# Optimization experiments

Measured on AMD Instinct MI355X. Metric: run time of the kernel, lower is better.

Reference implementation:

```python
import jax, jax.numpy as jnp
import numpy as np

N_NODES = 100000
N_EDGES = 640000
D_FEAT = 128
N_HIDDEN = 32


def setup_inputs() -> dict:
    key = jax.random.key(0)
    ks = jax.random.split(key, 8)
    x = jax.random.normal(ks[0], (N_NODES, D_FEAT), dtype=jnp.float32)
    edge_index = jax.random.randint(ks[1], (2, N_EDGES), 0, N_NODES, dtype=jnp.int64)
    # Glorot-ish scaled params
    W1_l = jax.random.normal(ks[2], (D_FEAT, N_HIDDEN), dtype=jnp.float32) / np.sqrt(D_FEAT)
    W1_r = jax.random.normal(ks[3], (D_FEAT, N_HIDDEN), dtype=jnp.float32) / np.sqrt(D_FEAT)
    b1 = jnp.zeros((N_HIDDEN,), dtype=jnp.float32)
    W2_l = jax.random.normal(ks[4], (N_HIDDEN, 1), dtype=jnp.float32) / np.sqrt(N_HIDDEN)
    W2_r = jax.random.normal(ks[5], (N_HIDDEN, 1), dtype=jnp.float32) / np.sqrt(N_HIDDEN)
    b2 = jnp.zeros((1,), dtype=jnp.float32)
    return {"x": x, "edge_index": edge_index, "W1_l": W1_l, "W1_r": W1_r,
            "b1": b1, "W2_l": W2_l, "W2_r": W2_r, "b2": b2}


def _sage_conv(h, src, dst, n_nodes, W_l, W_r, b):
    # mean aggregation of source features at destination nodes (PyG SAGEConv default)
    msg_sum = jax.ops.segment_sum(h[src], dst, num_segments=n_nodes)          # [N, d]
    deg = jax.ops.segment_sum(jnp.ones_like(src, dtype=h.dtype), dst,
                              num_segments=n_nodes)                           # [N]
    mean = msg_sum / jnp.maximum(deg, 1.0)[:, None]
    return mean @ W_l + h @ W_r + b


def reference(x, edge_index, W1_l, W1_r, b1, W2_l, W2_r, b2):
    src, dst = edge_index[0], edge_index[1]
    n = x.shape[0]
    h = jax.nn.relu(_sage_conv(x, src, dst, n, W1_l, W1_r, b1))
    # dropout p=0.1 is identity at inference (training=False)
    out = _sage_conv(h, src, dst, n, W2_l, W2_r, b2)
    return out  # [N, 1] node logits
```

## Files before the change

kernel.cpp:

```cpp
#include <hip/hip_runtime.h>

#define NN 100000
#define NE 640000
#define DF 128
#define NH 32
#define CAP 32
#define BINS 1563
#define BCAP 768
#define HBLK 256
#define EPB 2500
#define NTILE 6250
#define GEMMB 1563

typedef __attribute__((ext_vector_type(8))) short bf16x8;
typedef __attribute__((ext_vector_type(4))) float f32x4;

__device__ __forceinline__ unsigned short f2bf(float x) {
    union { float f; unsigned u; } c; c.f = x;
    unsigned r = c.u + 0x7fffu + ((c.u >> 16) & 1u);
    return (unsigned short)(r >> 16);
}
__device__ __forceinline__ float bf2f(unsigned short b) {
    union { unsigned u; float f; } c; c.u = ((unsigned)b) << 16;
    return c.f;
}

__global__ __launch_bounds__(256) void gemm_hist_kernel(
    const float* __restrict__ x, const float* __restrict__ W1_l,
    const float* __restrict__ W1_r, unsigned short* __restrict__ xl_bf,
    unsigned short* __restrict__ xr_bf, const int* __restrict__ dst,
    int* __restrict__ histmat)
{
    __shared__ unsigned short wl[8192];

    if (blockIdx.x >= GEMMB) {
        int* lh = (int*)wl;
        const int h = blockIdx.x - GEMMB;
        for (int b = threadIdx.x; b < BINS; b += 256) lh[b] = 0;
        __syncthreads();
        const int e0 = h * EPB;
        for (int i = threadIdx.x; i < EPB; i += 256)
            atomicAdd(&lh[dst[e0 + i] >> 6], 1);
        __syncthreads();
        for (int b = threadIdx.x; b < BINS; b += 256)
            histmat[b * HBLK + h] = lh[b];
        return;
    }

    for (int s = threadIdx.x; s < 1024; s += 256) {
        int lane = s & 63;
        int nt = (s >> 6) & 3;
        int ks = s >> 8;
        int n = nt * 16 + (lane & 15);
        const float* Wc = (n < 32) ? (W1_l + n) : (W1_r + (n - 32));
        unsigned short v[8];
#pragma unroll
        for (int i = 0; i < 8; i++) {
            int k = ks * 32 + ((i >> 2) << 4) + ((lane >> 4) << 2) + (i & 3);
            v[i] = f2bf(Wc[(size_t)k * 32]);
        }
        unsigned u0 = (unsigned)v[0] | ((unsigned)v[1] << 16);
        unsigned u1 = (unsigned)v[2] | ((unsigned)v[3] << 16);
        unsigned u2 = (unsigned)v[4] | ((unsigned)v[5] << 16);
        unsigned u3 = (unsigned)v[6] | ((unsigned)v[7] << 16);
        *(uint4*)&wl[s * 8] = make_uint4(u0, u1, u2, u3);
    }
    __syncthreads();

    const int lane = threadIdx.x & 63;
    const int tile = (blockIdx.x << 2) + (threadIdx.x >> 6);
    if (tile >= NTILE) return;
    const int m = lane & 15, g = lane >> 4;
    const int row0 = tile << 4;

#define BLOAD(ks, nt) const bf16x8 b##ks##nt = *(const bf16x8*)&wl[(((ks)*4 + (nt)) * 64 + lane) * 8];
    BLOAD(0,0) BLOAD(0,1) BLOAD(0,2) BLOAD(0,3)
    BLOAD(1,0) BLOAD(1,1) BLOAD(1,2) BLOAD(1,3)
    BLOAD(2,0) BLOAD(2,1) BLOAD(2,2) BLOAD(2,3)
    BLOAD(3,0) BLOAD(3,1) BLOAD(3,2) BLOAD(3,3)
#undef BLOAD

    f32x4 acc0 = {0.f,0.f,0.f,0.f}, acc1 = {0.f,0.f,0.f,0.f};
    f32x4 acc2 = {0.f,0.f,0.f,0.f}, acc3 = {0.f,0.f,0.f,0.f};

    const float* xp = x + (size_t)(row0 + m) * DF + g * 4;

#define KSTEP(ks) { \
    float4 fa = *(const float4*)(xp + (ks) * 32); \
    float4 fb = *(const float4*)(xp + (ks) * 32 + 16); \
    bf16x8 af; \
    af[0] = (short)f2bf(fa.x); af[1] = (short)f2bf(fa.y); \
    af[2] = (short)f2bf(fa.z); af[3] = (short)f2bf(fa.w); \
    af[4] = (short)f2bf(fb.x); af[5] = (short)f2bf(fb.y); \
    af[6] = (short)f2bf(fb.z); af[7] = (short)f2bf(fb.w); \
    acc0 = __builtin_amdgcn_mfma_f32_16x16x32_bf16(af, b##ks##0, acc0, 0, 0, 0); \
    acc1 = __builtin_amdgcn_mfma_f32_16x16x32_bf16(af, b##ks##1, acc1, 0, 0, 0); \
    acc2 = __builtin_amdgcn_mfma_f32_16x16x32_bf16(af, b##ks##2, acc2, 0, 0, 0); \
    acc3 = __builtin_amdgcn_mfma_f32_16x16x32_bf16(af, b##ks##3, acc3, 0, 0, 0); }
    KSTEP(0) KSTEP(1) KSTEP(2) KSTEP(3)
#undef KSTEP

#define CSTORE(nt) { \
    int n = (nt) * 16 + m; \
_Pragma("unroll") \
    for (int r = 0; r < 4; r++) { \
        int rr = row0 + g * 4 + r; \
        unsigned short v = f2bf(acc##nt[r]); \
        if (n < 32) xl_bf[(size_t)rr * 32 + n] = v; \
        else        xr_bf[(size_t)rr * 32 + (n - 32)] = v; \
    } }
    CSTORE(0) CSTORE(1) CSTORE(2) CSTORE(3)
#undef CSTORE
}

__global__ __launch_bounds__(256) void scan_kernel(const int* __restrict__ histmat,
                                                   int* __restrict__ startmat,
                                                   int* __restrict__ len)
{
    __shared__ int ls[256];
    const int j = blockIdx.x, t = threadIdx.x;
    int h = histmat[j * HBLK + t];
    ls[t] = h;
    __syncthreads();
    for (int off = 1; off < 256; off <<= 1) {
        int v = (t >= off) ? ls[t - off] : 0;
        __syncthreads();
        ls[t] += v;
        __syncthreads();
    }
    startmat[j * HBLK + t] = ls[t] - h;
    if (t == 255) len[j] = ls[255];
}

__global__ __launch_bounds__(256) void scatter_kernel(const int* __restrict__ src,
                                                      const int* __restrict__ dst,
                                                      const int* __restrict__ startmat,
                                                      int* __restrict__ binned)
{
    __shared__ int lhist[BINS];
    const int h = blockIdx.x;
    for (int b = threadIdx.x; b < BINS; b += 256) lhist[b] = 0;
    __syncthreads();
    const int e0 = h * EPB;
    for (int i = threadIdx.x; i < EPB; i += 256) {
        int s = src[e0 + i], d = dst[e0 + i];
        int bin = d >> 6;
        int lr = atomicAdd(&lhist[bin], 1);
        int pos = bin * BCAP + startmat[bin * HBLK + h] + lr;
        binned[pos] = (s << 6) | (d & 63);
    }
}

__global__ __launch_bounds__(256) void agg1_bin_kernel(
    const int* __restrict__ binned, const int* __restrict__ len,
    const unsigned short* __restrict__ xl_bf, const unsigned short* __restrict__ xr_bf,
    const float* __restrict__ b1, const float* __restrict__ W2_l,
    const float* __restrict__ W2_r, float* __restrict__ h2l, float* __restrict__ hrp)
{
    __shared__ int lcnt[64];
    __shared__ int lesrc[64 * CAP];
    const int j = blockIdx.x, t = threadIdx.x;
    if (t < 64) lcnt[t] = 0;
    __syncthreads();
    const int L = len[j];
    const int* seg = binned + (size_t)j * BCAP;
    for (int i = t; i < L; i += 256) {
        int pk = seg[i];
        int dl = pk & 63, s = pk >> 6;
        int p = atomicAdd(&lcnt[dl], 1);
        if (p < CAP) lesrc[(dl << 5) + p] = s;
    }
    __syncthreads();

    const int l = t & 31, grp = t >> 5;
    const int j8 = l >> 2, c = l & 3;
    const float4* b14 = (const float4*)&b1[c * 8];
    float4 bb0 = b14[0], bb1 = b14[1];
    const float4* wl4 = (const float4*)&W2_l[c * 8];
    float4 wl0 = wl4[0], wl1 = wl4[1];
    const float4* wr4 = (const float4*)&W2_r[c * 8];
    float4 wr0 = wr4[0], wr1 = wr4[1];
    const float bs[8]  = {bb0.x, bb0.y, bb0.z, bb0.w, bb1.x, bb1.y, bb1.z, bb1.w};
    const float wls[8] = {wl0.x, wl0.y, wl0.z, wl0.w, wl1.x, wl1.y, wl1.z, wl1.w};
    const float wrs[8] = {wr0.x, wr0.y, wr0.z, wr0.w, wr1.x, wr1.y, wr1.z, wr1.w};

    for (int dl = grp; dl < 64; dl += 8) {
        const int node = j * 64 + dl;
        if (node >= NN) break;
        const int dg = lcnt[dl];
        const int lim = (dg < CAP) ? dg : CAP;

        float acc[8];
#pragma unroll
        for (int i = 0; i < 8; i++) acc[i] = 0.f;

        for (int jb = 0; jb < lim; jb += 8) {
            int jj = jb + j8;
            if (jj < lim) {
                int s = lesrc[(dl << 5) + jj];
                uint4 v = *(const uint4*)&xl_bf[(size_t)s * NH + c * 8];
#pragma unroll
                for (int i = 0; i < 4; i++) {
                    unsigned u = (&v.x)[i];
                    acc[2 * i]     += bf2f((unsigned short)(u & 0xffffu));
                    acc[2 * i + 1] += bf2f((unsigned short)(u >> 16));
                }
            }
        }
#pragma unroll
        for (int mm = 4; mm <= 16; mm <<= 1)
#pragma unroll
            for (int i = 0; i < 8; i++) acc[i] += __shfl_xor(acc[i], mm);

        const float inv = 1.0f / fmaxf((float)dg, 1.0f);
        uint4 xv = *(const uint4*)&xr_bf[(size_t)node * NH + c * 8];
        float sl = 0.f, sr = 0.f;
#pragma unroll
        for (int i = 0; i < 4; i++) {
            unsigned u = (&xv.x)[i];
            float xlo = bf2f((unsigned short)(u & 0xffffu));
            float xhi = bf2f((unsigned short)(u >> 16));
            float h0 = fmaxf(fmaf(acc[2 * i],     inv, xlo + bs[2 * i]),     0.f);
            float h1 = fmaxf(fmaf(acc[2 * i + 1], inv, xhi + bs[2 * i + 1]), 0.f);
            sl = fmaf(h0, wls[2 * i], sl); sl = fmaf(h1, wls[2 * i + 1], sl);
            sr = fmaf(h0, wrs[2 * i], sr); sr = fmaf(h1, wrs[2 * i + 1], sr);
        }
        sl += __shfl_xor(sl, 1); sl += __shfl_xor(sl, 2);
        sr += __shfl_xor(sr, 1); sr += __shfl_xor(sr, 2);
        if (l == 0) {
            h2l[node] = sl;
            hrp[node] = sr;
        }
    }
}

__global__ __launch_bounds__(256) void agg2_bin_kernel(
    const int* __restrict__ binned, const int* __restrict__ len,
    const float* __restrict__ h2l, const float* __restrict__ hrp,
    const float* __restrict__ b2, float* __restrict__ out)
{
    __shared__ float lsum[64];
    __shared__ int lcc[64];
    const int j = blockIdx.x, t = threadIdx.x;
    if (t < 64) { lsum[t] = 0.f; lcc[t] = 0; }
    __syncthreads();
    const int L = len[j];
    const int* seg = binned + (size_t)j * BCAP;
    for (int i = t; i < L; i += 256) {
        int pk = seg[i];
        int dl = pk & 63, s = pk >> 6;
        atomicAdd(&lsum[dl], h2l[s]);
        atomicAdd(&lcc[dl], 1);
    }
    __syncthreads();
    if (t < 64) {
        int node = j * 64 + t;
        if (node < NN)
            out[node] = lsum[t] / fmaxf((float)lcc[t], 1.0f) + hrp[node] + b2[0];
    }
}

extern "C" void kernel_launch(void* const* d_in, const int* in_sizes, int n_in,
                              void* d_out, int out_size, void* d_ws, size_t ws_size,
                              hipStream_t stream)
{
    const float* x    = (const float*)d_in[0];
    const int*   ei   = (const int*)d_in[1];
    const float* W1_l = (const float*)d_in[2];
    const float* W1_r = (const float*)d_in[3];
    const float* b1   = (const float*)d_in[4];
    const float* W2_l = (const float*)d_in[5];
    const float* W2_r = (const float*)d_in[6];
    const float* b2   = (const float*)d_in[7];
    float* out = (float*)d_out;

    const int* src = ei;
    const int* dst = ei + NE;

    unsigned short* xl_bf = (unsigned short*)d_ws;
    unsigned short* xr_bf = xl_bf + (size_t)NN * NH;
    float* h2l      = (float*)(xr_bf + (size_t)NN * NH);
    float* hrp      = h2l + NN;
    int*   histmat  = (int*)(hrp + NN);
    int*   startmat = histmat + (size_t)BINS * HBLK;
    int*   len      = startmat + (size_t)BINS * HBLK;
    int*   binned   = len + BINS;

    gemm_hist_kernel<<<GEMMB + HBLK, 256, 0, stream>>>(x, W1_l, W1_r, xl_bf, xr_bf,
                                                       dst, histmat);
    scan_kernel<<<BINS, 256, 0, stream>>>(histmat, startmat, len);
    scatter_kernel<<<HBLK, 256, 0, stream>>>(src, dst, startmat, binned);
    agg1_bin_kernel<<<BINS, 256, 0, stream>>>(binned, len, xl_bf, xr_bf,
                                              b1, W2_l, W2_r, h2l, hrp);
    agg2_bin_kernel<<<BINS, 256, 0, stream>>>(binned, len, h2l, hrp, b2, out);
}
```

Baseline: 71.22 us.

## Drop scan kernel; compute bin offsets inside scatter and lengths in aggregators

```diff
diff --git a/kernel.cpp b/kernel.cpp
--- a/kernel.cpp
+++ b/kernel.cpp
@@ -7,8 +7,8 @@
 #define CAP 32
 #define BINS 1563
 #define BCAP 768
-#define HBLK 256
-#define EPB 2500
+#define HBLK 64
+#define EPB 10000
 #define NTILE 6250
 #define GEMMB 1563
 
@@ -113,56 +113,50 @@
 #undef CSTORE
 }
 
-__global__ __launch_bounds__(256) void scan_kernel(const int* __restrict__ histmat,
-                                                   int* __restrict__ startmat,
-                                                   int* __restrict__ len)
-{
-    __shared__ int ls[256];
-    const int j = blockIdx.x, t = threadIdx.x;
-    int h = histmat[j * HBLK + t];
-    ls[t] = h;
-    __syncthreads();
-    for (int off = 1; off < 256; off <<= 1) {
-        int v = (t >= off) ? ls[t - off] : 0;
-        __syncthreads();
-        ls[t] += v;
-        __syncthreads();
-    }
-    startmat[j * HBLK + t] = ls[t] - h;
-    if (t == 255) len[j] = ls[255];
-}
-
 __global__ __launch_bounds__(256) void scatter_kernel(const int* __restrict__ src,
                                                       const int* __restrict__ dst,
-                                                      const int* __restrict__ startmat,
+                                                      const int* __restrict__ histmat,
                                                       int* __restrict__ binned)
 {
-    __shared__ int lhist[BINS];
+    __shared__ int lstart[BINS];
+    __shared__ int lrank[BINS];
     const int h = blockIdx.x;
-    for (int b = threadIdx.x; b < BINS; b += 256) lhist[b] = 0;
+    for (int b = threadIdx.x; b < BINS; b += 256) {
+        const int* hr = histmat + b * HBLK;
+        int s = 0;
+        for (int hp = 0; hp < h; hp++) s += hr[hp];
+        lstart[b] = b * BCAP + s;
+        lrank[b] = 0;
+    }
     __syncthreads();
     const int e0 = h * EPB;
     for (int i = threadIdx.x; i < EPB; i += 256) {
         int s = src[e0 + i], d = dst[e0 + i];
         int bin = d >> 6;
-        int lr = atomicAdd(&lhist[bin], 1);
-        int pos = bin * BCAP + startmat[bin * HBLK + h] + lr;
-        binned[pos] = (s << 6) | (d & 63);
+        int lr = atomicAdd(&lrank[bin], 1);
+        binned[lstart[bin] + lr] = (s << 6) | (d & 63);
     }
 }
 
 __global__ __launch_bounds__(256) void agg1_bin_kernel(
-    const int* __restrict__ binned, const int* __restrict__ len,
+    const int* __restrict__ binned, const int* __restrict__ histmat,
     const unsigned short* __restrict__ xl_bf, const unsigned short* __restrict__ xr_bf,
     const float* __restrict__ b1, const float* __restrict__ W2_l,
     const float* __restrict__ W2_r, float* __restrict__ h2l, float* __restrict__ hrp)
 {
     __shared__ int lcnt[64];
     __shared__ int lesrc[64 * CAP];
+    __shared__ int Lsh;
     const int j = blockIdx.x, t = threadIdx.x;
-    if (t < 64) lcnt[t] = 0;
-    __syncthreads();
-    const int L = len[j];
+    if (t < 64) {
+        lcnt[t] = 0;
+        int v = histmat[j * HBLK + t];
+#pragma unroll
+        for (int mm = 1; mm < 64; mm <<= 1) v += __shfl_xor(v, mm);
+        if (t == 0) Lsh = v;
+    }
+    __syncthreads();
+    const int L = Lsh;
     const int* seg = binned + (size_t)j * BCAP;
     for (int i = t; i < L; i += 256) {
         int pk = seg[i];
@@ -235,16 +229,23 @@
 }
 
 __global__ __launch_bounds__(256) void agg2_bin_kernel(
-    const int* __restrict__ binned, const int* __restrict__ len,
+    const int* __restrict__ binned, const int* __restrict__ histmat,
     const float* __restrict__ h2l, const float* __restrict__ hrp,
     const float* __restrict__ b2, float* __restrict__ out)
 {
     __shared__ float lsum[64];
     __shared__ int lcc[64];
+    __shared__ int Lsh;
     const int j = blockIdx.x, t = threadIdx.x;
-    if (t < 64) { lsum[t] = 0.f; lcc[t] = 0; }
-    __syncthreads();
-    const int L = len[j];
+    if (t < 64) {
+        lsum[t] = 0.f; lcc[t] = 0;
+        int v = histmat[j * HBLK + t];
+#pragma unroll
+        for (int mm = 1; mm < 64; mm <<= 1) v += __shfl_xor(v, mm);
+        if (t == 0) Lsh = v;
+    }
+    __syncthreads();
+    const int L = Lsh;
     const int* seg = binned + (size_t)j * BCAP;
     for (int i = t; i < L; i += 256) {
         int pk = seg[i];
@@ -282,15 +283,12 @@
     float* h2l      = (float*)(xr_bf + (size_t)NN * NH);
     float* hrp      = h2l + NN;
     int*   histmat  = (int*)(hrp + NN);
-    int*   startmat = histmat + (size_t)BINS * HBLK;
-    int*   len      = startmat + (size_t)BINS * HBLK;
-    int*   binned   = len + BINS;
+    int*   binned   = histmat + (size_t)BINS * HBLK;
 
     gemm_hist_kernel<<<GEMMB + HBLK, 256, 0, stream>>>(x, W1_l, W1_r, xl_bf, xr_bf,
                                                        dst, histmat);
-    scan_kernel<<<BINS, 256, 0, stream>>>(histmat, startmat, len);
-    scatter_kernel<<<HBLK, 256, 0, stream>>>(src, dst, startmat, binned);
-    agg1_bin_kernel<<<BINS, 256, 0, stream>>>(binned, len, xl_bf, xr_bf,
+    scatter_kernel<<<HBLK, 256, 0, stream>>>(src, dst, histmat, binned);
+    agg1_bin_kernel<<<BINS, 256, 0, stream>>>(binned, histmat, xl_bf, xr_bf,
                                               b1, W2_l, W2_r, h2l, hrp);
-    agg2_bin_kernel<<<BINS, 256, 0, stream>>>(binned, len, h2l, hrp, b2, out);
-}
+    agg2_bin_kernel<<<BINS, 256, 0, stream>>>(binned, histmat, h2l, hrp, b2, out);
+}
```

After: 102.2 us. +43.5%, slower.

## Fuse edge binning into GEMM kernel with block-local sort and drop scan/scatter

Applied to the files above, without the earlier changes.

```diff
diff --git a/kernel.cpp b/kernel.cpp
--- a/kernel.cpp
+++ b/kernel.cpp
@@ -6,7 +6,6 @@
 #define NH 32
 #define CAP 32
 #define BINS 1563
-#define BCAP 768
 #define HBLK 256
 #define EPB 2500
 #define NTILE 6250
@@ -25,25 +24,50 @@
     return c.f;
 }
 
-__global__ __launch_bounds__(256) void gemm_hist_kernel(
+__global__ __launch_bounds__(256) void gemm_sort_kernel(
     const float* __restrict__ x, const float* __restrict__ W1_l,
     const float* __restrict__ W1_r, unsigned short* __restrict__ xl_bf,
-    unsigned short* __restrict__ xr_bf, const int* __restrict__ dst,
-    int* __restrict__ histmat)
+    unsigned short* __restrict__ xr_bf, const int* __restrict__ src,
+    const int* __restrict__ dst, int2* __restrict__ packmat,
+    int* __restrict__ binned)
 {
     __shared__ unsigned short wl[8192];
+    __shared__ int lpart[256];
 
     if (blockIdx.x >= GEMMB) {
-        int* lh = (int*)wl;
+        int* lhist = (int*)wl;
         const int h = blockIdx.x - GEMMB;
-        for (int b = threadIdx.x; b < BINS; b += 256) lh[b] = 0;
-        __syncthreads();
+        const int t = threadIdx.x;
         const int e0 = h * EPB;
-        for (int i = threadIdx.x; i < EPB; i += 256)
-            atomicAdd(&lh[dst[e0 + i] >> 6], 1);
-        __syncthreads();
-        for (int b = threadIdx.x; b < BINS; b += 256)
-            histmat[b * HBLK + h] = lh[b];
+        for (int b = t; b < BINS; b += 256) lhist[b] = 0;
+        __syncthreads();
+        for (int i = t; i < EPB; i += 256)
+            atomicAdd(&lhist[dst[e0 + i] >> 6], 1);
+        __syncthreads();
+        const int k0 = t * 7, k1 = (k0 + 7 < BINS) ? k0 + 7 : BINS;
+        int s = 0;
+        for (int k = k0; k < k1; k++) s += lhist[k];
+        lpart[t] = s;
+        __syncthreads();
+        for (int off = 1; off < 256; off <<= 1) {
+            int v = (t >= off) ? lpart[t - off] : 0;
+            __syncthreads();
+            lpart[t] += v;
+            __syncthreads();
+        }
+        int run = lpart[t] - s;
+        for (int k = k0; k < k1; k++) {
+            int c = lhist[k];
+            packmat[(size_t)h * BINS + k] = make_int2(run, c);
+            lhist[k] = run;
+            run += c;
+        }
+        __syncthreads();
+        for (int i = t; i < EPB; i += 256) {
+            int sv = src[e0 + i], d = dst[e0 + i];
+            int pos = atomicAdd(&lhist[d >> 6], 1);
+            binned[e0 + pos] = (sv << 6) | (d & 63);
+        }
         return;
     }
 
@@ -113,64 +137,41 @@
 #undef CSTORE
 }
 
-__global__ __launch_bounds__(256) void scan_kernel(const int* __restrict__ histmat,
-                                                   int* __restrict__ startmat,
-                                                   int* __restrict__ len)
-{
-    __shared__ int ls[256];
-    const int j = blockIdx.x, t = threadIdx.x;
-    int h = histmat[j * HBLK + t];
-    ls[t] = h;
-    __syncthreads();
-    for (int off = 1; off < 256; off <<= 1) {
-        int v = (t >= off) ? ls[t - off] : 0;
-        __syncthreads();
-        ls[t] += v;
-        __syncthreads();
-    }
-    startmat[j * HBLK + t] = ls[t] - h;
-    if (t == 255) len[j] = ls[255];
-}
-
-__global__ __launch_bounds__(256) void scatter_kernel(const int* __restrict__ src,
-                                                      const int* __restrict__ dst,
-                                                      const int* __restrict__ startmat,
-                                                      int* __restrict__ binned)
-{
-    __shared__ int lhist[BINS];
-    const int h = blockIdx.x;
-    for (int b = threadIdx.x; b < BINS; b += 256) lhist[b] = 0;
-    __syncthreads();
-    const int e0 = h * EPB;
-    for (int i = threadIdx.x; i < EPB; i += 256) {
-        int s = src[e0 + i], d = dst[e0 + i];
-        int bin = d >> 6;
-        int lr = atomicAdd(&lhist[bin], 1);
-        int pos = bin * BCAP + startmat[bin * HBLK + h] + lr;
-        binned[pos] = (s << 6) | (d & 63);
-    }
-}
-
 __global__ __launch_bounds__(256) void agg1_bin_kernel(
-    const int* __restrict__ binned, const int* __restrict__ len,
+    const int* __restrict__ binned, const int2* __restrict__ packmat,
     const unsigned short* __restrict__ xl_bf, const unsigned short* __restrict__ xr_bf,
     const float* __restrict__ b1, const float* __restrict__ W2_l,
-    const float* __restrict__ W2_r, float* __restrict__ h2l, float* __restrict__ hrp)
+    const float* __restrict__ W2_r, float* __restrict__ h2l, float* __restrict__ hrp,
+    int* __restrict__ esrc, int* __restrict__ deg)
 {
     __shared__ int lcnt[64];
     __shared__ int lesrc[64 * CAP];
     const int j = blockIdx.x, t = threadIdx.x;
     if (t < 64) lcnt[t] = 0;
     __syncthreads();
-    const int L = len[j];
-    const int* seg = binned + (size_t)j * BCAP;
-    for (int i = t; i < L; i += 256) {
-        int pk = seg[i];
-        int dl = pk & 63, s = pk >> 6;
-        int p = atomicAdd(&lcnt[dl], 1);
-        if (p < CAP) lesrc[(dl << 5) + p] = s;
+
+    {
+        int2 sc = packmat[(size_t)t * BINS + j];
+        const int base = t * EPB + sc.x;
+        for (int k = 0; k < sc.y; k++) {
+            int pk = binned[base + k];
+            int dl = pk & 63, s = pk >> 6;
+            int p = atomicAdd(&lcnt[dl], 1);
+            if (p < CAP) lesrc[(dl << 5) + p] = s;
+        }
     }
     __syncthreads();
+
+    for (int i = t; i < 64 * CAP; i += 256) {
+        int node = j * 64 + (i >> 5);
+        int c = lcnt[i >> 5];
+        if (node < NN && (i & 31) < ((c < CAP) ? c : CAP))
+            esrc[(size_t)node * CAP + (i & 31)] = lesrc[i];
+    }
+    if (t < 64) {
+        int node = j * 64 + t;
+        if (node < NN) deg[node] = lcnt[t];
+    }
 
     const int l = t & 31, grp = t >> 5;
     const int j8 = l >> 2, c = l & 3;
@@ -234,30 +235,27 @@
     }
 }
 
-__global__ __launch_bounds__(256) void agg2_bin_kernel(
-    const int* __restrict__ binned, const int* __restrict__ len,
+__global__ __launch_bounds__(256) void agg2_final_kernel(
+    const int* __restrict__ deg, const int* __restrict__ esrc,
     const float* __restrict__ h2l, const float* __restrict__ hrp,
     const float* __restrict__ b2, float* __restrict__ out)
 {
-    __shared__ float lsum[64];
-    __shared__ int lcc[64];
-    const int j = blockIdx.x, t = threadIdx.x;
-    if (t < 64) { lsum[t] = 0.f; lcc[t] = 0; }
-    __syncthreads();
-    const int L = len[j];
-    const int* seg = binned + (size_t)j * BCAP;
-    for (int i = t; i < L; i += 256) {
-        int pk = seg[i];
-        int dl = pk & 63, s = pk >> 6;
-        atomicAdd(&lsum[dl], h2l[s]);
-        atomicAdd(&lcc[dl], 1);
-    }
-    __syncthreads();
-    if (t < 64) {
-        int node = j * 64 + t;
-        if (node < NN)
-            out[node] = lsum[t] / fmaxf((float)lcc[t], 1.0f) + hrp[node] + b2[0];
-    }
+    int i = blockIdx.x * 256 + threadIdx.x;
+    if (i >= NN) return;
+    int dg = deg[i];
+    int lim = (dg < CAP) ? dg : CAP;
+    const int* ep = esrc + (size_t)i * CAP;
+    float s0 = 0.f, s1 = 0.f, s2 = 0.f, s3 = 0.f;
+    int j = 0;
+    for (; j + 3 < lim; j += 4) {
+        int4 s = *(const int4*)&ep[j];
+        s0 += h2l[s.x];
+        s1 += h2l[s.y];
+        s2 += h2l[s.z];
+        s3 += h2l[s.w];
+    }
+    for (; j < lim; j++) s0 += h2l[ep[j]];
+    out[i] = ((s0 + s1) + (s2 + s3)) / fmaxf((float)dg, 1.0f) + hrp[i] + b2[0];
 }
 
 extern "C" void kernel_launch(void* const* d_in, const int* in_sizes, int n_in,
@@ -281,16 +279,14 @@
     unsigned short* xr_bf = xl_bf + (size_t)NN * NH;
     float* h2l      = (float*)(xr_bf + (size_t)NN * NH);
     float* hrp      = h2l + NN;
-    int*   histmat  = (int*)(hrp + NN);
-    int*   startmat = histmat + (size_t)BINS * HBLK;
-    int*   len      = startmat + (size_t)BINS * HBLK;
-    int*   binned   = len + BINS;
-
-    gemm_hist_kernel<<<GEMMB + HBLK, 256, 0, stream>>>(x, W1_l, W1_r, xl_bf, xr_bf,
-                                                       dst, histmat);
-    scan_kernel<<<BINS, 256, 0, stream>>>(histmat, startmat, len);
-    scatter_kernel<<<HBLK, 256, 0, stream>>>(src, dst, startmat, binned);
-    agg1_bin_kernel<<<BINS, 256, 0, stream>>>(binned, len, xl_bf, xr_bf,
-                                              b1, W2_l, W2_r, h2l, hrp);
-    agg2_bin_kernel<<<BINS, 256, 0, stream>>>(binned, len, h2l, hrp, b2, out);
-}
+    int2*  packmat  = (int2*)(hrp + NN);
+    int*   binned   = (int*)(packmat + (size_t)HBLK * BINS);
+    int*   esrc     = binned + NE;
+    int*   deg      = esrc + (size_t)NN * CAP;
+
+    gemm_sort_kernel<<<GEMMB + HBLK, 256, 0, stream>>>(x, W1_l, W1_r, xl_bf, xr_bf,
+                                                       src, dst, packmat, binned);
+    agg1_bin_kernel<<<BINS, 256, 0, stream>>>(binned, packmat, xl_bf, xr_bf,
+                                              b1, W2_l, W2_r, h2l, hrp, esrc, deg);
+    agg2_final_kernel<<<(NN + 255) / 256, 256, 0, stream>>>(deg, esrc, h2l, hrp, b2, out);
+}
```

Measured after the change: 67.06 us. -5.8%, faster.
